# Performance work log

Measured on AMD Instinct MI355X. Metric: run time of the kernel, lower is better.

Reference implementation:

```python
import jax, jax.numpy as jnp
import numpy as np

N_NODES = 50000
D_FEAT = 512
H1, H2 = 128, 64
N_CLASSES = 40
E_MP = 800000
E_LP = 250000


def gcn_conv(x, W, b, edge_index, edge_weight, num_nodes):
    """PyG GCNConv: add self-loops, symmetric norm D^-1/2 (A+I) D^-1/2, then (norm-agg)(xW)+b."""
    row, col = edge_index[0], edge_index[1]
    loop = jnp.arange(num_nodes)
    row = jnp.concatenate([row, loop])
    col = jnp.concatenate([col, loop])
    ew = jnp.concatenate([edge_weight, jnp.ones((num_nodes,), x.dtype)])
    deg = jax.ops.segment_sum(ew, col, num_segments=num_nodes)
    dinv = jnp.where(deg > 0, deg ** -0.5, 0.0).astype(x.dtype)
    norm = dinv[row] * ew * dinv[col]  # [E+N]
    h = x @ W  # [N, out]
    msg = h[row] * norm[:, None]  # gather + scale per edge
    out = jax.ops.segment_sum(msg, col, num_segments=num_nodes) + b
    return out


def setup_inputs() -> dict:
    key = jax.random.key(0)
    ks = jax.random.split(key, 16)
    inp = {}
    inp["x"] = jax.random.normal(ks[0], (N_NODES, D_FEAT), jnp.float32)
    inp["train_pos_edge_index"] = jax.random.randint(ks[1], (2, E_MP), 0, N_NODES)
    inp["edge_index"] = jax.random.randint(ks[2], (2, E_MP), 0, N_NODES)
    inp["edge_weight"] = jax.random.uniform(ks[3], (E_MP,), jnp.float32)
    inp["pos_edge_index"] = jax.random.randint(ks[4], (2, E_LP), 0, N_NODES)
    inp["neg_edge_index"] = jax.random.randint(ks[5], (2, E_LP), 0, N_NODES)
    # parameters (glorot-ish scaled)
    def w(k, i, o):
        return jax.random.normal(k, (i, o), jnp.float32) * (2.0 / (i + o)) ** 0.5
    inp["W1"] = w(ks[6], D_FEAT, H1)
    inp["b1"] = jnp.zeros((H1,), jnp.float32)
    inp["W2"] = w(ks[7], H1, H2)
    inp["b2"] = jnp.zeros((H2,), jnp.float32)
    inp["W_attr"] = w(ks[8], H2, N_CLASSES)
    inp["b_attr"] = jnp.zeros((N_CLASSES,), jnp.float32)
    inp["W_att"] = w(ks[9], H2, N_CLASSES)
    inp["b_att"] = jnp.zeros((N_CLASSES,), jnp.float32)
    return inp


def reference(x, train_pos_edge_index, edge_index, edge_weight, pos_edge_index,
              neg_edge_index, W1, b1, W2, b2, W_attr, b_attr, W_att, b_att):
    ones = jnp.ones((train_pos_edge_index.shape[1],), x.dtype)
    h = jax.nn.relu(gcn_conv(x, W1, b1, train_pos_edge_index, ones, N_NODES))
    h = gcn_conv(h, W2, b2, train_pos_edge_index, ones, N_NODES)  # [N, 64]
    attr = gcn_conv(h, W_attr, b_attr, edge_index, edge_weight, N_NODES)
    # gradient reversal is identity in forward
    att = gcn_conv(h, W_att, b_att, edge_index, edge_weight, N_NODES)
    total = jnp.concatenate([pos_edge_index, neg_edge_index], axis=-1)  # [2, 2*E_LP]
    x_j = h[total[0]]
    x_i = h[total[1]]
    res = jnp.einsum("ef,ef->e", x_i, x_j)
    return res, jax.nn.log_softmax(attr, axis=1), jax.nn.log_softmax(att, axis=1)
```

## Files before the change

### kernel.cpp

```cpp
#include <hip/hip_runtime.h>

typedef short s16x8 __attribute__((ext_vector_type(8)));
typedef short s16x4 __attribute__((ext_vector_type(4)));
typedef float f32x4 __attribute__((ext_vector_type(4)));

static __device__ __forceinline__ unsigned short f2bf(float f) {
  unsigned u = __float_as_uint(f);
  u += 0x7fff + ((u >> 16) & 1);
  return (unsigned short)(u >> 16);
}
static __device__ __forceinline__ float bf2f(unsigned short h) {
  return __uint_as_float(((unsigned)h) << 16);
}


static __global__ void k_init(int* cntT, int* cntE, int n) {
  int i = blockIdx.x * blockDim.x + threadIdx.x;
  if (i < n) { cntT[i] = 0; cntE[i] = 0; }
}

static __global__ void k_count(const int* __restrict__ tcol, const int* __restrict__ ecol,
                               int* __restrict__ cntT, int* __restrict__ cntE,
                               int* __restrict__ rankT, int* __restrict__ rankE, int E) {
  int e = blockIdx.x * blockDim.x + threadIdx.x;
  if (e < E) {
    rankT[e] = atomicAdd(&cntT[tcol[e]], 1);
    rankE[e] = atomicAdd(&cntE[ecol[e]], 1);
  }
}

static __global__ __launch_bounds__(256) void k_scanA(
    const int* __restrict__ cntT, const int* __restrict__ cntE,
    int* __restrict__ bsum, int n, int nb) {
  const int* cnt = blockIdx.y ? cntE : cntT;
  int tid = threadIdx.x;
  int base = blockIdx.x * 1024 + tid * 4;
  int s = 0;
#pragma unroll
  for (int q = 0; q < 4; ++q) { int i = base + q; if (i < n) s += cnt[i]; }
  __shared__ int red[256];
  red[tid] = s;
  __syncthreads();
  for (int off = 128; off > 0; off >>= 1) {
    if (tid < off) red[tid] += red[tid + off];
    __syncthreads();
  }
  if (tid == 0) bsum[blockIdx.y * nb + blockIdx.x] = red[0];
}

static __global__ void k_scanB(int* bsum, int* ptrT, int* ptrE, int nb, int n) {
  int a = threadIdx.x;
  if (a > 1) return;
  int* bs = bsum + a * nb;
  int run = 0;
  for (int i = 0; i < nb; ++i) { int c = bs[i]; bs[i] = run; run += c; }
  (a ? ptrE : ptrT)[n] = run;
}

static __global__ __launch_bounds__(256) void k_scanC(
    const int* __restrict__ cntT, const int* __restrict__ cntE,
    const int* __restrict__ bsum, int* __restrict__ ptrT, int* __restrict__ ptrE,
    int n, int nb) {
  const int* cnt = blockIdx.y ? cntE : cntT;
  int* ptr = blockIdx.y ? ptrE : ptrT;
  int tid = threadIdx.x;
  int pre = bsum[blockIdx.y * nb + blockIdx.x];
  int base = blockIdx.x * 1024 + tid * 4;
  int v[4];
  int s = 0;
#pragma unroll
  for (int q = 0; q < 4; ++q) { int i = base + q; v[q] = (i < n) ? cnt[i] : 0; s += v[q]; }
  __shared__ int red[256];
  red[tid] = s;
  __syncthreads();
  for (int off = 1; off < 256; off <<= 1) {
    int t = (tid >= off) ? red[tid - off] : 0;
    __syncthreads();
    red[tid] += t;
    __syncthreads();
  }
  int run = pre + (tid ? red[tid - 1] : 0);
#pragma unroll
  for (int q = 0; q < 4; ++q) {
    int i = base + q;
    if (i < n) ptr[i] = run;
    run += v[q];
  }
}

static __global__ void k_fill(const int* __restrict__ trow, const int* __restrict__ tcol,
                              const int* __restrict__ erow, const int* __restrict__ ecol,
                              const float* __restrict__ ew,
                              const int* __restrict__ ptrT, const int* __restrict__ ptrE,
                              const int* __restrict__ rankT, const int* __restrict__ rankE,
                              int* __restrict__ srcT, int2* __restrict__ srcwE, int E) {
  int e = blockIdx.x * blockDim.x + threadIdx.x;
  if (e >= E) return;
  srcT[ptrT[tcol[e]] + rankT[e]] = trow[e];
  int2 p;
  p.x = erow[e];
  p.y = __float_as_int(ew[e]);
  srcwE[ptrE[ecol[e]] + rankE[e]] = p;
}

static __global__ void k_dinv2(const int* __restrict__ cntT, const int2* __restrict__ srcwE,
                               const int* __restrict__ ptrE,
                               float* __restrict__ dinvT, float* __restrict__ dinvE, int n) {
  int i = blockIdx.x * blockDim.x + threadIdx.x;
  if (i >= n) return;
  dinvT[i] = rsqrtf((float)cntT[i] + 1.0f);
  float s = 1.0f;
  int e = ptrE[i + 1];
  for (int j = ptrE[i]; j < e; ++j) s += __int_as_float(srcwE[j].y);
  dinvE[i] = rsqrtf(s);
}


static __global__ void k_cvtW(const float* __restrict__ W, unsigned short* __restrict__ Wh,
                              unsigned short* __restrict__ Wl, int K, int Nc) {
  int t = blockIdx.x * blockDim.x + threadIdx.x;
  if (t >= K * Nc) return;
  int k = t / Nc, c = t - k * Nc;
  float v = W[t];
  unsigned short hi = f2bf(v);
  Wh[(size_t)c * K + k] = hi;
  Wl[(size_t)c * K + k] = f2bf(v - bf2f(hi));
}


#define PADU 56

static __global__ __launch_bounds__(256) void k_gemm_mfma_split(
    const float* __restrict__ A, const unsigned short* __restrict__ Bh,
    const unsigned short* __restrict__ Bl, float* __restrict__ C, int M, int K) {
  __shared__ __align__(16) unsigned short Ah[128][PADU];
  __shared__ __align__(16) unsigned short Al[128][PADU];
  __shared__ __align__(16) unsigned short Bsh[128][PADU];
  __shared__ __align__(16) unsigned short Bsl[128][PADU];
  int tid = threadIdx.x;
  int lane = tid & 63, wid = tid >> 6;
  int wr = wid >> 1, wc = wid & 1;
  int l15 = lane & 15, l4 = lane >> 4;
  int brow = blockIdx.x * 128;
  f32x4 acc[4][4] = {};

  for (int k0 = 0; k0 < K; k0 += 32) {
    __syncthreads();
#pragma unroll
    for (int q = 0; q < 4; ++q) {
      int idx = tid + q * 256;
      int r = idx >> 3, c4 = (idx & 7) * 4;
      int gr = brow + r;
      float4 v = (gr < M) ? *(const float4*)&A[(size_t)gr * K + k0 + c4]
                          : make_float4(0.f, 0.f, 0.f, 0.f);
      unsigned short h0 = f2bf(v.x), h1 = f2bf(v.y), h2 = f2bf(v.z), h3 = f2bf(v.w);
      s16x4 hv = {(short)h0, (short)h1, (short)h2, (short)h3};
      s16x4 lv = {(short)f2bf(v.x - bf2f(h0)), (short)f2bf(v.y - bf2f(h1)),
                  (short)f2bf(v.z - bf2f(h2)), (short)f2bf(v.w - bf2f(h3))};
      *(s16x4*)&Ah[r][c4] = hv;
      *(s16x4*)&Al[r][c4] = lv;
    }
#pragma unroll
    for (int q = 0; q < 2; ++q) {
      int idx = tid + q * 256;
      int r = idx >> 2, c8 = (idx & 3) * 8;
      *(s16x8*)&Bsh[r][c8] = *(const s16x8*)&Bh[(size_t)r * K + k0 + c8];
      *(s16x8*)&Bsl[r][c8] = *(const s16x8*)&Bl[(size_t)r * K + k0 + c8];
    }
    __syncthreads();
    s16x8 afh[4], afl[4], bfh[4], bfl[4];
#pragma unroll
    for (int m = 0; m < 4; ++m) {
      int r = wr * 64 + m * 16 + l15;
      afh[m] = *(const s16x8*)&Ah[r][l4 * 8];
      afl[m] = *(const s16x8*)&Al[r][l4 * 8];
    }
#pragma unroll
    for (int n = 0; n < 4; ++n) {
      int c = wc * 64 + n * 16 + l15;
      bfh[n] = *(const s16x8*)&Bsh[c][l4 * 8];
      bfl[n] = *(const s16x8*)&Bsl[c][l4 * 8];
    }
#pragma unroll
    for (int m = 0; m < 4; ++m)
#pragma unroll
      for (int n = 0; n < 4; ++n) {
        acc[m][n] = __builtin_amdgcn_mfma_f32_16x16x32_bf16(afh[m], bfh[n], acc[m][n], 0, 0, 0);
        acc[m][n] = __builtin_amdgcn_mfma_f32_16x16x32_bf16(afl[m], bfh[n], acc[m][n], 0, 0, 0);
        acc[m][n] = __builtin_amdgcn_mfma_f32_16x16x32_bf16(afh[m], bfl[n], acc[m][n], 0, 0, 0);
      }
  }
#pragma unroll
  for (int m = 0; m < 4; ++m) {
    int rbase = brow + wr * 64 + m * 16 + l4 * 4;
#pragma unroll
    for (int n = 0; n < 4; ++n) {
      int c = wc * 64 + n * 16 + l15;
#pragma unroll
      for (int j = 0; j < 4; ++j) {
        int r = rbase + j;
        if (r < M) C[(size_t)r * 128 + c] = acc[m][n][j];
      }
    }
  }
}


template <int F, bool RELU, bool WEIGHTED>
static __global__ __launch_bounds__(256) void k_gather4(
    const float* __restrict__ H, const int* __restrict__ rowptr,
    const int* __restrict__ src, const int2* __restrict__ srcw,
    const float* __restrict__ dinv, const float* __restrict__ Hpre,
    const float* __restrict__ bias, float* __restrict__ out, int n) {
  const int L = F / 4;
  int node = blockIdx.x * (256 / L) + threadIdx.x / L;
  if (node >= n) return;
  int f4 = (threadIdx.x % L) * 4;
  float d = dinv[node];
  float4 hp = *(const float4*)&Hpre[(size_t)node * F + f4];
  float ax = hp.x * d, ay = hp.y * d, az = hp.z * d, aw = hp.w * d;
  int j = rowptr[node], e = rowptr[node + 1];
  for (; j + 1 < e; j += 2) {
    int r0, r1;
    float w0, w1;
    if (WEIGHTED) {
      int2 a = srcw[j], b = srcw[j + 1];
      r0 = a.x; r1 = b.x;
      w0 = dinv[r0] * __int_as_float(a.y);
      w1 = dinv[r1] * __int_as_float(b.y);
    } else {
      r0 = src[j]; r1 = src[j + 1];
      w0 = dinv[r0]; w1 = dinv[r1];
    }
    float4 v0 = *(const float4*)&H[(size_t)r0 * F + f4];
    float4 v1 = *(const float4*)&H[(size_t)r1 * F + f4];
    ax += v0.x * w0 + v1.x * w1;
    ay += v0.y * w0 + v1.y * w1;
    az += v0.z * w0 + v1.z * w1;
    aw += v0.w * w0 + v1.w * w1;
  }
  if (j < e) {
    int r;
    float wj;
    if (WEIGHTED) { int2 a = srcw[j]; r = a.x; wj = dinv[r] * __int_as_float(a.y); }
    else { r = src[j]; wj = dinv[r]; }
    float4 v = *(const float4*)&H[(size_t)r * F + f4];
    ax += v.x * wj; ay += v.y * wj; az += v.z * wj; aw += v.w * wj;
  }
  float bx = 0, by = 0, bz = 0, bw = 0;
  if (bias) { float4 bb = *(const float4*)&bias[f4]; bx = bb.x; by = bb.y; bz = bb.z; bw = bb.w; }
  ax = ax * d + bx; ay = ay * d + by; az = az * d + bz; aw = aw * d + bw;
  if (RELU) { ax = fmaxf(ax, 0.f); ay = fmaxf(ay, 0.f); az = fmaxf(az, 0.f); aw = fmaxf(aw, 0.f); }
  float4 o; o.x = ax; o.y = ay; o.z = az; o.w = aw;
  *(float4*)&out[(size_t)node * F + f4] = o;
}


static __global__ __launch_bounds__(256) void k_gemm(
    const float* __restrict__ A, const float* __restrict__ B,
    const float* __restrict__ bias, float* __restrict__ C,
    int M, int N, int K) {
  const int BM = 64, BN = 64, BK = 16;
  __shared__ float As[BK][BM + 4];
  __shared__ float Bs[BK][BN + 4];
  int tid = threadIdx.x;
  int tr = tid >> 4, tc = tid & 15;
  int brow = blockIdx.y * BM, bcol = blockIdx.x * BN;
  float acc[4][4] = {};
  for (int k0 = 0; k0 < K; k0 += BK) {
#pragma unroll
    for (int i = tid; i < BM * BK; i += 256) {
      int m = i >> 4, kk = i & 15;
      int gr = brow + m;
      As[kk][m] = (gr < M) ? A[(size_t)gr * K + k0 + kk] : 0.f;
    }
#pragma unroll
    for (int i = tid; i < BK * BN; i += 256) {
      int kk = i >> 6, n = i & 63;
      int gc = bcol + n;
      Bs[kk][n] = (gc < N) ? B[(size_t)(k0 + kk) * N + gc] : 0.f;
    }
    __syncthreads();
#pragma unroll
    for (int kk = 0; kk < BK; ++kk) {
      float a[4], b[4];
#pragma unroll
      for (int i = 0; i < 4; ++i) a[i] = As[kk][tr * 4 + i];
#pragma unroll
      for (int j = 0; j < 4; ++j) b[j] = Bs[kk][tc * 4 + j];
#pragma unroll
      for (int i = 0; i < 4; ++i)
#pragma unroll
        for (int j = 0; j < 4; ++j) acc[i][j] += a[i] * b[j];
    }
    __syncthreads();
  }
#pragma unroll
  for (int i = 0; i < 4; ++i) {
    int r = brow + tr * 4 + i;
    if (r >= M) continue;
#pragma unroll
    for (int j = 0; j < 4; ++j) {
      int c = bcol + tc * 4 + j;
      if (c < N) C[(size_t)r * N + c] = acc[i][j] + (bias ? bias[c] : 0.f);
    }
  }
}


static __global__ void k_logsoftmax40(float* __restrict__ X, int n) {
  int i = blockIdx.x * blockDim.x + threadIdx.x;
  if (i >= n) return;
  float4 v[10];
#pragma unroll
  for (int q = 0; q < 10; ++q) v[q] = *(const float4*)&X[(size_t)i * 40 + q * 4];
  float m = -1e30f;
#pragma unroll
  for (int q = 0; q < 10; ++q)
    m = fmaxf(m, fmaxf(fmaxf(v[q].x, v[q].y), fmaxf(v[q].z, v[q].w)));
  float s = 0.f;
#pragma unroll
  for (int q = 0; q < 10; ++q)
    s += expf(v[q].x - m) + expf(v[q].y - m) + expf(v[q].z - m) + expf(v[q].w - m);
  float ls = logf(s) + m;
#pragma unroll
  for (int q = 0; q < 10; ++q) {
    float4 o; o.x = v[q].x - ls; o.y = v[q].y - ls; o.z = v[q].z - ls; o.w = v[q].w - ls;
    *(float4*)&X[(size_t)i * 40 + q * 4] = o;
  }
}


static __global__ __launch_bounds__(256) void k_linkpred4(
    const float* __restrict__ H2, const int* __restrict__ pos,
    const int* __restrict__ neg, float* __restrict__ res, int Elp) {
  int t = blockIdx.x * 256 + threadIdx.x;
  int e = t >> 4, f4 = (t & 15) * 4;
  if (e >= 2 * Elp) return;
  int a, b;
  if (e < Elp) { a = pos[e]; b = pos[Elp + e]; }
  else { int e2 = e - Elp; a = neg[e2]; b = neg[Elp + e2]; }
  float4 va = *(const float4*)&H2[(size_t)a * 64 + f4];
  float4 vb = *(const float4*)&H2[(size_t)b * 64 + f4];
  float p = va.x * vb.x + va.y * vb.y + va.z * vb.z + va.w * vb.w;
  p += __shfl_xor(p, 1);
  p += __shfl_xor(p, 2);
  p += __shfl_xor(p, 4);
  p += __shfl_xor(p, 8);
  if ((t & 15) == 0) res[e] = p;
}


extern "C" void kernel_launch(void* const* d_in, const int* in_sizes, int n_in,
                              void* d_out, int out_size, void* d_ws, size_t ws_size,
                              hipStream_t stream) {
  const float* x    = (const float*)d_in[0];
  const int*   tp   = (const int*)d_in[1];
  const int*   ei   = (const int*)d_in[2];
  const float* ew   = (const float*)d_in[3];
  const int*   pos  = (const int*)d_in[4];
  const int*   neg  = (const int*)d_in[5];
  const float* W1   = (const float*)d_in[6];
  const float* b1   = (const float*)d_in[7];
  const float* W2   = (const float*)d_in[8];
  const float* b2   = (const float*)d_in[9];
  const float* Wattr= (const float*)d_in[10];
  const float* battr= (const float*)d_in[11];
  const float* Watt = (const float*)d_in[12];
  const float* batt = (const float*)d_in[13];

  const int N   = in_sizes[0] / 512;
  const int EMP = in_sizes[1] / 2;
  const int ELP = in_sizes[4] / 2;
  const int NB  = (N + 1023) / 1024;

  float* ws = (float*)d_ws;
  float* dinvT = ws;
  float* dinvE = dinvT + N;
  int* rowptrT = (int*)(dinvE + N);
  int* rowptrE = rowptrT + (N + 4);
  int* srcT    = rowptrE + (N + 4);
  int2* srcwE  = (int2*)(srcT + EMP);
  int* bsum    = (int*)(srcwE + EMP);
  unsigned short* W1h = (unsigned short*)(bsum + 128);
  unsigned short* W1l = W1h + 512 * 128;
  float* bufA  = (float*)(W1l + 512 * 128);
  float* bufB  = bufA + (size_t)N * 128;
  float* bufC  = bufB + (size_t)N * 128;
  int* rankT = (int*)bufA;
  int* rankE = rankT + EMP;
  int* cntT  = (int*)bufB;
  int* cntE  = cntT + N;

  float* out_res  = (float*)d_out;
  float* out_attr = out_res + 2 * (size_t)ELP;
  float* out_att  = out_attr + (size_t)N * 40;

  dim3 b256(256);
  int gN = (N + 255) / 256;
  int gE = (EMP + 255) / 256;

  k_init<<<gN, b256, 0, stream>>>(cntT, cntE, N);
  k_cvtW<<<(512 * 128 + 255) / 256, b256, 0, stream>>>(W1, W1h, W1l, 512, 128);
  k_count<<<gE, b256, 0, stream>>>(tp + EMP, ei + EMP, cntT, cntE, rankT, rankE, EMP);
  {
    dim3 gs(NB, 2);
    k_scanA<<<gs, b256, 0, stream>>>(cntT, cntE, bsum, N, NB);
    k_scanB<<<1, 64, 0, stream>>>(bsum, rowptrT, rowptrE, NB, N);
    k_scanC<<<gs, b256, 0, stream>>>(cntT, cntE, bsum, rowptrT, rowptrE, N, NB);
  }
  k_fill<<<gE, b256, 0, stream>>>(tp, tp + EMP, ei, ei + EMP, ew,
                                  rowptrT, rowptrE, rankT, rankE, srcT, srcwE, EMP);
  k_dinv2<<<gN, b256, 0, stream>>>(cntT, srcwE, rowptrE, dinvT, dinvE, N);

  k_gemm_mfma_split<<<(N + 127) / 128, b256, 0, stream>>>(x, W1h, W1l, bufA, N, 512);
  k_gather4<128, true, false><<<(N + 7) / 8, b256, 0, stream>>>(
      bufA, rowptrT, srcT, nullptr, dinvT, bufA, b1, bufB, N);

  {
    dim3 grid(1, (N + 63) / 64);
    k_gemm<<<grid, b256, 0, stream>>>(bufB, W2, nullptr, bufA, N, 64, 128);
  }
  k_gather4<64, false, false><<<(N + 15) / 16, b256, 0, stream>>>(
      bufA, rowptrT, srcT, nullptr, dinvT, bufA, b2, bufC, N);

  k_gather4<64, false, true><<<(N + 15) / 16, b256, 0, stream>>>(
      bufC, rowptrE, nullptr, srcwE, dinvE, bufC, nullptr, bufA, N);

  {
    dim3 grid(1, (N + 63) / 64);
    k_gemm<<<grid, b256, 0, stream>>>(bufA, Wattr, battr, out_attr, N, 40, 64);
    k_gemm<<<grid, b256, 0, stream>>>(bufA, Watt, batt, out_att, N, 40, 64);
  }
  k_logsoftmax40<<<gN, b256, 0, stream>>>(out_attr, N);
  k_logsoftmax40<<<gN, b256, 0, stream>>>(out_att, N);

  k_linkpred4<<<(2 * ELP * 16 + 255) / 256, b256, 0, stream>>>(bufC, pos, neg, out_res, ELP);
}
```

Before: 432.5 us.

## Shrink MFMA GEMM tile to 64 rows, prefetch A in registers, read B directly

The first-layer split-bf16 GEMM now uses 64-row tiles instead of 128, which doubles the block count (about 782 blocks) for better occupancy across CUs. The next K-slice of A is loaded into registers while the current slice is converted and stored to LDS, overlapping global latency with compute. B fragments are read straight from global/L2 instead of being staged through shared memory, which cuts LDS use and one staging pass. The cost is less reuse of B per block and more global B traffic, though W1 is small and likely to stay cached.

```diff
diff --git a/kernel.cpp b/kernel.cpp
--- a/kernel.cpp
+++ b/kernel.cpp
@@ -128,61 +128,72 @@
 }
 
 
-#define PADU 56
+#define PADU 36
 
 static __global__ __launch_bounds__(256) void k_gemm_mfma_split(
     const float* __restrict__ A, const unsigned short* __restrict__ Bh,
     const unsigned short* __restrict__ Bl, float* __restrict__ C, int M, int K) {
-  __shared__ __align__(16) unsigned short Ah[128][PADU];
-  __shared__ __align__(16) unsigned short Al[128][PADU];
-  __shared__ __align__(16) unsigned short Bsh[128][PADU];
-  __shared__ __align__(16) unsigned short Bsl[128][PADU];
+  __shared__ __align__(16) unsigned short Ah[64][PADU];
+  __shared__ __align__(16) unsigned short Al[64][PADU];
   int tid = threadIdx.x;
   int lane = tid & 63, wid = tid >> 6;
   int wr = wid >> 1, wc = wid & 1;
   int l15 = lane & 15, l4 = lane >> 4;
-  int brow = blockIdx.x * 128;
-  f32x4 acc[4][4] = {};
+  int brow = blockIdx.x * 64;
+  f32x4 acc[2][4] = {};
+
+  float4 v[2];
+#pragma unroll
+  for (int q = 0; q < 2; ++q) {
+    int idx = tid + q * 256;
+    int r = idx >> 3, c4 = (idx & 7) * 4;
+    int gr = brow + r;
+    v[q] = (gr < M) ? *(const float4*)&A[(size_t)gr * K + c4]
+                    : make_float4(0.f, 0.f, 0.f, 0.f);
+  }
 
   for (int k0 = 0; k0 < K; k0 += 32) {
     __syncthreads();
 #pragma unroll
-    for (int q = 0; q < 4; ++q) {
+    for (int q = 0; q < 2; ++q) {
       int idx = tid + q * 256;
       int r = idx >> 3, c4 = (idx & 7) * 4;
-      int gr = brow + r;
-      float4 v = (gr < M) ? *(const float4*)&A[(size_t)gr * K + k0 + c4]
-                          : make_float4(0.f, 0.f, 0.f, 0.f);
-      unsigned short h0 = f2bf(v.x), h1 = f2bf(v.y), h2 = f2bf(v.z), h3 = f2bf(v.w);
+      float4 w = v[q];
+      unsigned short h0 = f2bf(w.x), h1 = f2bf(w.y), h2 = f2bf(w.z), h3 = f2bf(w.w);
       s16x4 hv = {(short)h0, (short)h1, (short)h2, (short)h3};
-      s16x4 lv = {(short)f2bf(v.x - bf2f(h0)), (short)f2bf(v.y - bf2f(h1)),
-                  (short)f2bf(v.z - bf2f(h2)), (short)f2bf(v.w - bf2f(h3))};
+      s16x4 lv = {(short)f2bf(w.x - bf2f(h0)), (short)f2bf(w.y - bf2f(h1)),
+                  (short)f2bf(w.z - bf2f(h2)), (short)f2bf(w.w - bf2f(h3))};
       *(s16x4*)&Ah[r][c4] = hv;
       *(s16x4*)&Al[r][c4] = lv;
     }
-#pragma unroll
-    for (int q = 0; q < 2; ++q) {
-      int idx = tid + q * 256;
-      int r = idx >> 2, c8 = (idx & 3) * 8;
-      *(s16x8*)&Bsh[r][c8] = *(const s16x8*)&Bh[(size_t)r * K + k0 + c8];
-      *(s16x8*)&Bsl[r][c8] = *(const s16x8*)&Bl[(size_t)r * K + k0 + c8];
-    }
-    __syncthreads();
-    s16x8 afh[4], afl[4], bfh[4], bfl[4];
-#pragma unroll
-    for (int m = 0; m < 4; ++m) {
-      int r = wr * 64 + m * 16 + l15;
+    if (k0 + 32 < K) {
+#pragma unroll
+      for (int q = 0; q < 2; ++q) {
+        int idx = tid + q * 256;
+        int r = idx >> 3, c4 = (idx & 7) * 4;
+        int gr = brow + r;
+        v[q] = (gr < M) ? *(const float4*)&A[(size_t)gr * K + k0 + 32 + c4]
+                        : make_float4(0.f, 0.f, 0.f, 0.f);
+      }
+    }
+    __syncthreads();
+
+    s16x8 afh[2], afl[2];
+#pragma unroll
+    for (int m = 0; m < 2; ++m) {
+      int r = wr * 32 + m * 16 + l15;
       afh[m] = *(const s16x8*)&Ah[r][l4 * 8];
       afl[m] = *(const s16x8*)&Al[r][l4 * 8];
     }
+    s16x8 bfh[4], bfl[4];
 #pragma unroll
     for (int n = 0; n < 4; ++n) {
       int c = wc * 64 + n * 16 + l15;
-      bfh[n] = *(const s16x8*)&Bsh[c][l4 * 8];
-      bfl[n] = *(const s16x8*)&Bsl[c][l4 * 8];
-    }
-#pragma unroll
-    for (int m = 0; m < 4; ++m)
+      bfh[n] = *(const s16x8*)&Bh[(size_t)c * K + k0 + l4 * 8];
+      bfl[n] = *(const s16x8*)&Bl[(size_t)c * K + k0 + l4 * 8];
+    }
+#pragma unroll
+    for (int m = 0; m < 2; ++m)
 #pragma unroll
       for (int n = 0; n < 4; ++n) {
         acc[m][n] = __builtin_amdgcn_mfma_f32_16x16x32_bf16(afh[m], bfh[n], acc[m][n], 0, 0, 0);
@@ -191,8 +202,8 @@
       }
   }
 #pragma unroll
-  for (int m = 0; m < 4; ++m) {
-    int rbase = brow + wr * 64 + m * 16 + l4 * 4;
+  for (int m = 0; m < 2; ++m) {
+    int rbase = brow + wr * 32 + m * 16 + l4 * 4;
 #pragma unroll
     for (int n = 0; n < 4; ++n) {
       int c = wc * 64 + n * 16 + l15;
@@ -413,7 +424,7 @@
                                   rowptrT, rowptrE, rankT, rankE, srcT, srcwE, EMP);
   k_dinv2<<<gN, b256, 0, stream>>>(cntT, srcwE, rowptrE, dinvT, dinvE, N);
 
-  k_gemm_mfma_split<<<(N + 127) / 128, b256, 0, stream>>>(x, W1h, W1l, bufA, N, 512);
+  k_gemm_mfma_split<<<(N + 63) / 64, b256, 0, stream>>>(x, W1h, W1l, bufA, N, 512);
   k_gather4<128, true, false><<<(N + 7) / 8, b256, 0, stream>>>(
       bufA, rowptrT, srcT, nullptr, dinvT, bufA, b1, bufB, N);
 
```

Result: slower. 455.6 us (+5.3%).
